# Optimization experiments

Hardware: AMD Instinct MI355X
Metric: run time of the kernel (lower is better)

Reference implementation:

```python
import jax, jax.numpy as jnp
import numpy as np
from jax import lax

SFREQ = 250.0
ORDER = 4
BANDS = [(4.0, 8.0), (8.0, 12.0), (12.0, 16.0), (16.0, 20.0), (20.0, 24.0), (24.0, 28.0), (28.0, 32.0), (32.0, 36.0), (36.0, 40.0)]
KLEN = int(SFREQ // 2)
if KLEN % 2 == 0:
    KLEN += 1  # 125 taps, odd -> same-length output with pad K//2


def _butter_bandpass(order, low, high, sfreq):
    # numpy reimplementation of scipy.signal.butter(order, [low,high]/nyq, btype='band')
    nyq = sfreq / 2.0
    fs = 2.0
    warped = 2.0 * fs * np.tan(np.pi * np.array([low, high]) / nyq / fs)
    m = np.arange(-order + 1, order, 2)
    p = -np.exp(1j * np.pi * m / (2 * order))  # analog Butterworth LP prototype poles
    k = 1.0
    bw = warped[1] - warped[0]
    wo = np.sqrt(warped[0] * warped[1])
    p_lp = p * bw / 2.0
    p_bp = np.concatenate([p_lp + np.sqrt(p_lp ** 2 - wo ** 2), p_lp - np.sqrt(p_lp ** 2 - wo ** 2)])
    z_bp = np.zeros(order, dtype=complex)
    k_bp = k * bw ** order
    fs2 = 2.0 * fs  # bilinear transform
    z_d = (fs2 + z_bp) / (fs2 - z_bp)
    p_d = (fs2 + p_bp) / (fs2 - p_bp)
    z_d = np.append(z_d, -np.ones(len(p_bp) - len(z_bp)))
    k_d = k_bp * np.real(np.prod(fs2 - z_bp) / np.prod(fs2 - p_bp))
    b = np.real(k_d * np.poly(z_d))
    a = np.real(np.poly(p_d))
    return b, a


def _make_kernel(low, high):
    # IIR impulse response (centered impulse, as in the torch module), Hann window, L1 normalize
    b, a = _butter_bandpass(ORDER, low, high, SFREQ)
    x = np.zeros(KLEN)
    x[KLEN // 2] = 1.0
    h = np.zeros(KLEN)
    for n in range(KLEN):
        s = 0.0
        for i in range(len(b)):
            if n - i >= 0:
                s += b[i] * x[n - i]
        for j in range(1, len(a)):
            if n - j >= 0:
                s -= a[j] * h[n - j]
        h[n] = s / a[0]
    nn = np.arange(KLEN)
    h = h * (0.5 - 0.5 * np.cos(2.0 * np.pi * nn / (KLEN - 1)))  # symmetric Hann
    return h / np.sum(np.abs(h))


def setup_inputs() -> dict:
    key = jax.random.key(0)
    x = jax.random.normal(key, (64, 64, 1000), dtype=jnp.float32)  # (B, C, T) EEG
    kernels = jnp.asarray(np.stack([_make_kernel(lo, hi) for lo, hi in BANDS]), dtype=jnp.float32)  # (n_bands, K)
    return {"x": x, "kernels": kernels}


def reference(x, kernels):
    # out[b, i, c, t] = cross-correlation of channel c with band-i kernel (torch Conv1d semantics)
    B, C, T = x.shape
    nb, K = kernels.shape
    pad = K // 2
    x2 = x.reshape(B * C, 1, T)
    w = kernels[:, None, :]  # (n_bands, 1, K)
    y = lax.conv_general_dilated(x2, w, (1,), [(pad, pad)], dimension_numbers=("NCH", "OIH", "NCH"))
    return y.reshape(B, C, nb, T).transpose(0, 2, 1, 3)  # (B, n_bands, C, T)
```

## Files before the change

kernel.cpp:

```cpp
#include <hip/hip_runtime.h>
#include <hip/hip_bf16.h>


#define T_LEN    1000
#define NB       9
#define S_COPY   1160
#define SLOTS    145
#define STG_W    264

typedef __attribute__((ext_vector_type(8))) short short8;
typedef __attribute__((ext_vector_type(4))) float f32x4;

__device__ __forceinline__ unsigned int f2bf(float f) {
    union { __hip_bfloat16 h; unsigned short u; } cv;
    cv.h = __float2bfloat16(f);
    return (unsigned int)cv.u;
}

__global__ __launch_bounds__(256) void fbank_mfma(
    const float* __restrict__ x,
    const float* __restrict__ kern,
    float* __restrict__ out)
{
    __shared__ unsigned short xs[8 * S_COPY];

    const int tid = threadIdx.x;
    const int bc  = blockIdx.x;
    const int b   = bc >> 6, c = bc & 63;
    const float* xrow = x + (size_t)bc * T_LEN;

    {
        const int r = tid >> 5, q0 = tid & 31;
        #pragma unroll
        for (int i = 0; i < 5; ++i) {
            int q = q0 + 32 * i;
            if (q < SLOTS) {
                int idx0 = 8 * q + r - 64;
                unsigned int d[4];
                #pragma unroll
                for (int e2 = 0; e2 < 4; ++e2) {
                    int i0 = idx0 + 2 * e2, i1 = i0 + 1;
                    float v0 = ((unsigned)i0 < T_LEN) ? xrow[i0] : 0.f;
                    float v1 = ((unsigned)i1 < T_LEN) ? xrow[i1] : 0.f;
                    d[e2] = f2bf(v0) | (f2bf(v1) << 16);
                }
                *reinterpret_cast<uint4*>(&xs[r * S_COPY + 8 * q]) =
                    make_uint4(d[0], d[1], d[2], d[3]);
            }
        }
    }

    const int lane = tid & 63;
    const int wid  = tid >> 6;
    const int n = lane & 15, g = lane >> 4;

    short8 bt[4];
    #pragma unroll
    for (int kk = 0; kk < 4; ++kk) {
        unsigned int u[4];
        #pragma unroll
        for (int e2 = 0; e2 < 4; ++e2) {
            int k0 = kk * 32 + 8 * g + 2 * e2;
            float v0 = (n < NB && k0 < 125)     ? kern[n * 125 + k0]     : 0.f;
            float v1 = (n < NB && k0 + 1 < 125) ? kern[n * 125 + k0 + 1] : 0.f;
            u[e2] = f2bf(v0) | (f2bf(v1) << 16);
        }
        union { uint4 u4; short8 s8; } cv;
        cv.u4 = make_uint4(u[0], u[1], u[2], u[3]);
        bt[kk] = cv.s8;
    }

    __syncthreads();

    const int t0w = wid << 8;
    const int rl  = (n + 2) & 7;
    const char* xsb = reinterpret_cast<const char*>(xs);
    const int LB = 2 * (1159 * rl + 2 + n + 8 * g + t0w);

    short8 F[8];
    #pragma unroll
    for (int u = 0; u < 6; ++u)
        F[u] = *reinterpret_cast<const short8*>(xsb + LB + 32 * u);

    f32x4 acc[16];
    #pragma unroll
    for (int m = 0; m < 16; ++m) {
        F[(m + 6) & 7] = *reinterpret_cast<const short8*>(xsb + LB + 32 * (m + 6));
        f32x4 a = {0.f, 0.f, 0.f, 0.f};
        #pragma unroll
        for (int kk = 0; kk < 4; ++kk)
            a = __builtin_amdgcn_mfma_f32_16x16x32_bf16(F[(m + 2 * kk) & 7], bt[kk], a, 0, 0, 0);
        acc[m] = a;
    }

    float* stg = reinterpret_cast<float*>(xs);
    for (int w = 0; w < 4; ++w) {
        __syncthreads();
        if (wid == w) {
            if (n < NB) {
                #pragma unroll
                for (int m = 0; m < 16; ++m)
                    *reinterpret_cast<f32x4*>(stg + n * STG_W + 16 * m + 4 * g) = acc[m];
            }
            const int tl = 4 * lane;
            const bool ok = (t0w + tl + 4 <= T_LEN);
            #pragma unroll
            for (int i = 0; i < NB; ++i) {
                f32x4 v = *reinterpret_cast<const f32x4*>(stg + i * STG_W + tl);
                if (ok)
                    *reinterpret_cast<f32x4*>(
                        out + ((size_t)(b * NB + i) * 64 + c) * T_LEN + t0w + tl) = v;
            }
        }
    }
}

extern "C" void kernel_launch(void* const* d_in, const int* in_sizes, int n_in,
                              void* d_out, int out_size, void* d_ws, size_t ws_size,
                              hipStream_t stream) {
    const float* x    = (const float*)d_in[0];
    const float* kern = (const float*)d_in[1];
    float* out = (float*)d_out;

    fbank_mfma<<<64 * 64, 256, 0, stream>>>(x, kern, out);
}
```

Measured before the change: 62.21 us.

## Precompute bf16 filter taps in a prep kernel and swizzle block order

Adds a tiny one-block kernel that converts the filter taps to padded bf16 once in workspace, so each main block loads its MFMA B operand with four 16-byte loads instead of 32 scalar loads plus conversions. It also remaps block index so consecutive blocks span different batch/channel groups, changing the order in which output rows are written. The cost is an extra kernel launch, and the main kernel now depends on workspace contents that prep_taps writes.

```diff
diff --git a/kernel.cpp b/kernel.cpp
--- a/kernel.cpp
+++ b/kernel.cpp
@@ -4,6 +4,7 @@
 
 #define T_LEN    1000
 #define NB       9
+#define KP       128
 #define S_COPY   1160
 #define SLOTS    145
 #define STG_W    264
@@ -17,15 +18,28 @@
     return (unsigned int)cv.u;
 }
 
+__global__ __launch_bounds__(256) void prep_taps(const float* __restrict__ kern,
+                                                 unsigned short* __restrict__ kwb) {
+    const int t = threadIdx.x;
+    #pragma unroll
+    for (int i = 0; i < 8; ++i) {
+        int idx = t + 256 * i;
+        int band = idx >> 7, k = idx & 127;
+        float v = (band < NB && k < 125) ? kern[band * 125 + k] : 0.f;
+        kwb[idx] = (unsigned short)f2bf(v);
+    }
+}
+
 __global__ __launch_bounds__(256) void fbank_mfma(
     const float* __restrict__ x,
-    const float* __restrict__ kern,
+    const unsigned short* __restrict__ kwb,
     float* __restrict__ out)
 {
     __shared__ unsigned short xs[8 * S_COPY];
 
     const int tid = threadIdx.x;
-    const int bc  = blockIdx.x;
+    const int bid = blockIdx.x;
+    const int bc  = ((bid & 7) << 9) + (bid >> 3);
     const int b   = bc >> 6, c = bc & 63;
     const float* xrow = x + (size_t)bc * T_LEN;
 
@@ -56,19 +70,8 @@
 
     short8 bt[4];
     #pragma unroll
-    for (int kk = 0; kk < 4; ++kk) {
-        unsigned int u[4];
-        #pragma unroll
-        for (int e2 = 0; e2 < 4; ++e2) {
-            int k0 = kk * 32 + 8 * g + 2 * e2;
-            float v0 = (n < NB && k0 < 125)     ? kern[n * 125 + k0]     : 0.f;
-            float v1 = (n < NB && k0 + 1 < 125) ? kern[n * 125 + k0 + 1] : 0.f;
-            u[e2] = f2bf(v0) | (f2bf(v1) << 16);
-        }
-        union { uint4 u4; short8 s8; } cv;
-        cv.u4 = make_uint4(u[0], u[1], u[2], u[3]);
-        bt[kk] = cv.s8;
-    }
+    for (int kk = 0; kk < 4; ++kk)
+        bt[kk] = *reinterpret_cast<const short8*>(kwb + n * KP + kk * 32 + g * 8);
 
     __syncthreads();
 
@@ -121,6 +124,8 @@
     const float* x    = (const float*)d_in[0];
     const float* kern = (const float*)d_in[1];
     float* out = (float*)d_out;
+    unsigned short* kwb = (unsigned short*)d_ws;
 
-    fbank_mfma<<<64 * 64, 256, 0, stream>>>(x, kern, out);
+    prep_taps<<<1, 256, 0, stream>>>(kern, kwb);
+    fbank_mfma<<<64 * 64, 256, 0, stream>>>(x, kwb, out);
 }
```

Measured after the change: 56.20 us. 1.11x faster.
